# Optimization experiments

Measured on AMD Instinct MI355X. Metric: run time of the kernel, lower is better.

Reference implementation:

```python
import jax, jax.numpy as jnp
import numpy as np

B, V, M, H = 256, 128, 256, 1024
TIMING_DIM = 10          # ceil(log2(max_timesteps=1024))
DECAY_ALPHA = 0.99
IN_DIM = (V + TIMING_DIM + 1 + 1) * M  # 35840


def setup_inputs() -> dict:
    key = jax.random.key(0)
    ks = jax.random.split(key, 12)
    x = jax.random.uniform(ks[0], (B, V), dtype=jnp.float32)
    memory = jax.random.uniform(ks[1], (B, M, V), dtype=jnp.float32)
    memory_timings = jax.random.randint(ks[2], (B, M), 0, 1000).astype(jnp.int64)
    memory_surprise = jax.random.uniform(ks[3], (B, M), dtype=jnp.float32)
    last_prediction = jax.random.uniform(ks[4], (B, V), dtype=jnp.float32)
    s1 = 1.0 / np.sqrt(IN_DIM)
    s2 = 1.0 / np.sqrt(H)
    W1 = jax.random.uniform(ks[5], (IN_DIM, H), dtype=jnp.float32, minval=-s1, maxval=s1)
    b1 = jnp.zeros((H,), jnp.float32)
    Wg = jax.random.uniform(ks[6], (IN_DIM, H), dtype=jnp.float32, minval=-s1, maxval=s1)
    bg = jnp.zeros((H,), jnp.float32)
    W2 = jax.random.uniform(ks[7], (H, V), dtype=jnp.float32, minval=-s2, maxval=s2)
    b2 = jnp.zeros((V,), jnp.float32)
    return {"x": x, "memory": memory, "memory_timings": memory_timings,
            "memory_surprise": memory_surprise, "last_prediction": last_prediction,
            "W1": W1, "b1": b1, "Wg": Wg, "bg": bg, "W2": W2, "b2": b2}


def _step(x, memory, memory_timings, memory_surprise, last_prediction):
    # surprise of incoming token under last prediction
    surprise = -jnp.log(jnp.sum(x * last_prediction, axis=1) + 1e-8)  # [B]
    # age + decay
    timings = memory_timings + 1
    surp = memory_surprise * DECAY_ALPHA
    # ring-buffer roll, write newest at slot 0
    mem = jnp.roll(memory, 1, axis=1).at[:, 0, :].set(x)
    timings = jnp.roll(timings, 1, axis=1).at[:, 0].set(0)
    surp = jnp.roll(surp, 1, axis=1).at[:, 0].set(surprise)
    # sort by age ascending, gather memory/surprise
    idx = jnp.argsort(timings, axis=1)                               # [B,M]
    sorted_timings = jnp.take_along_axis(timings, idx, axis=1)       # [B,M]
    sorted_memory = jnp.take_along_axis(mem, idx[..., None], axis=1)  # [B,M,V]
    sorted_surprise = jnp.take_along_axis(surp, idx, axis=1)          # [B,M]
    # binary encode timings
    powers = 2 ** jnp.arange(TIMING_DIM, dtype=sorted_timings.dtype)
    bits = ((sorted_timings[..., None] // powers) % 2).astype(jnp.float32)  # [B,M,T]
    norm_t = sorted_timings.astype(jnp.float32) / (
        jnp.max(sorted_timings, axis=1, keepdims=True).astype(jnp.float32) + 1.0)
    pred_input = jnp.concatenate(
        [sorted_memory.reshape(B, -1), bits.reshape(B, -1),
         norm_t.reshape(B, -1), sorted_surprise.reshape(B, -1)], axis=1)  # [B, IN_DIM]
    return pred_input


def reference(x, memory, memory_timings, memory_surprise, last_prediction,
              W1, b1, Wg, bg, W2, b2):
    pred_input = _step(x, memory, memory_timings, memory_surprise, last_prediction)
    # gated dense network: h = (xW1+b1) * sigmoid(xWg+bg); logits = hW2+b2
    h = (pred_input @ W1 + b1) * jax.nn.sigmoid(pred_input @ Wg + bg)
    return h @ W2 + b2
```

## Files before the change

### kernel.cpp

```cpp
#include <hip/hip_runtime.h>
#include <stdint.h>
#include <math.h>

#define BB 256
#define VV 128
#define MM 256
#define TDIM 10
#define HH 1024
#define IN_DIM 35840
#define KSPLIT 16
#define KSLICE 2240
#define BK 32
#define NCHUNK 70

using f32x4  = __attribute__((ext_vector_type(4))) float;
using bf16x8 = __attribute__((ext_vector_type(8))) short;

__device__ __forceinline__ unsigned short f2bf(float f) {
    unsigned int u = __float_as_uint(f);
    unsigned int r = (u + 0x7FFFu + ((u >> 16) & 1u)) >> 16;
    return (unsigned short)r;
}

__device__ __forceinline__ void gload_lds16(const void* g, void* l) {
    __builtin_amdgcn_global_load_lds(
        (const __attribute__((address_space(1))) unsigned int*)g,
        (__attribute__((address_space(3))) unsigned int*)l,
        16, 0, 0);
}

__global__ __launch_bounds__(256)
void k_build(const float* __restrict__ x, const float* __restrict__ memory,
             const int* __restrict__ timings, const float* __restrict__ msurp,
             const float* __restrict__ lastp, short* __restrict__ A)
{
    int b = blockIdx.x, t = threadIdx.x;
    __shared__ int t_s[MM], idx_s[MM], st_s[MM];
    __shared__ float red[MM];
    __shared__ float s_surprise;

    t_s[t] = (t == 0) ? 0 : timings[b*MM + t - 1] + 1;
    red[t] = (t < VV) ? x[b*VV + t] * lastp[b*VV + t] : 0.f;
    __syncthreads();
    for (int s = 128; s > 0; s >>= 1) {
        if (t < s) red[t] += red[t + s];
        __syncthreads();
    }
    if (t == 0) s_surprise = -logf(red[0] + 1e-8f);

    int ti = t_s[t], cnt = 0;
    #pragma unroll 4
    for (int j = 0; j < MM; ++j) {
        int tj = t_s[j];
        cnt += (tj < ti) || (tj == ti && j < t);
    }
    idx_s[cnt] = t;
    st_s[cnt]  = ti;
    __syncthreads();

    float invm = 1.f / ((float)st_s[MM-1] + 1.f);
    short* Ab = A + (size_t)b * IN_DIM;
    {
        int st = st_s[t], src = idx_s[t];
        #pragma unroll
        for (int tt = 0; tt < TDIM; ++tt)
            Ab[32768 + t*TDIM + tt] = (short)f2bf((float)((st >> tt) & 1));
        Ab[35328 + t] = (short)f2bf((float)st * invm);
        float sv = (src == 0) ? s_surprise : msurp[b*MM + src - 1] * 0.99f;
        Ab[35584 + t] = (short)f2bf(sv);
    }
    int half = t >> 7, v = t & (VV-1);
    for (int p = half; p < MM; p += 2) {
        int src = idx_s[p];
        float val = (src == 0) ? x[b*VV + v]
                               : memory[((size_t)b*MM + src - 1)*VV + v];
        Ab[p*VV + v] = (short)f2bf(val);
    }
}

__global__ __launch_bounds__(512, 4)
void k_gemm(const short* __restrict__ A, const float* __restrict__ W1,
            const float* __restrict__ Wg, float* __restrict__ P)
{
    int ks = blockIdx.x;
    int xt = blockIdx.y;
    const float* W = (xt < 16) ? W1 : Wg;
    int wcol0 = (xt & 15) * 64;
    int pcol0 = xt * 64;
    int k0 = ks * KSLICE;

    __shared__ bf16x8 As8[3][1024];
    __shared__ float  Wl[3][2048];

    int t = threadIdx.x;
    int l = t & 63, wv = t >> 6;
    int r = l & 15, q = l >> 4;
    int wm = wv & 3, nh = wv >> 2;

    int aoff[4];
    #pragma unroll
    for (int mt = 0; mt < 4; ++mt) {
        int R = wm*64 + mt*16 + r;
        aoff[mt] = R*4 + (q ^ ((R >> 1) & 3));
    }
    int ncol[2];
    #pragma unroll
    for (int nt = 0; nt < 2; ++nt) {
        int n = nh*32 + nt*16 + r;
        ncol[nt] = n ^ (q << 4);
    }

    f32x4 acc[4][2];
    #pragma unroll
    for (int mt = 0; mt < 4; ++mt)
        #pragma unroll
        for (int nt = 0; nt < 2; ++nt)
            acc[mt][nt] = (f32x4){0.f, 0.f, 0.f, 0.f};

    int wkk = t >> 4;
    int wnF = ((t & 15) * 4) ^ (((wkk >> 3) & 3) << 4);

#define STAGE(sbuf, cc) do {                                                  \
        int kc_ = k0 + (cc)*BK;                                               \
        {   int G_ = t;                                                       \
            int m_ = G_ >> 2;                                                 \
            int kb_ = (G_ & 3) ^ ((m_ >> 1) & 3);                             \
            gload_lds16(A + (size_t)m_*IN_DIM + kc_ + kb_*8,                  \
                        (char*)&As8[sbuf][0] + (size_t)(t & ~63)*16);         \
        }                                                                     \
        {   int G_ = t + 512;                                                 \
            int m_ = G_ >> 2;                                                 \
            int kb_ = (G_ & 3) ^ ((m_ >> 1) & 3);                             \
            gload_lds16(A + (size_t)m_*IN_DIM + kc_ + kb_*8,                  \
                        (char*)&As8[sbuf][0] + (size_t)((t & ~63) + 512)*16); \
        }                                                                     \
        gload_lds16(W + (size_t)(kc_ + wkk)*HH + wcol0 + wnF,                 \
                    (char*)&Wl[sbuf][0] + (size_t)(t & ~63)*16);              \
    } while (0)

    STAGE(0, 0);
    STAGE(1, 1);
    STAGE(2, 2);
    asm volatile("s_waitcnt vmcnt(6)" ::: "memory");
    __builtin_amdgcn_s_barrier();

    for (int c = 0; c < NCHUNK; ++c) {
        int buf = c % 3;

        bf16x8 af[4], bfr[2];
        #pragma unroll
        for (int mt = 0; mt < 4; ++mt) af[mt] = As8[buf][aoff[mt]];
        #pragma unroll
        for (int nt = 0; nt < 2; ++nt) {
            const float* wb = &Wl[buf][ncol[nt]];
            bf16x8 bb;
            #pragma unroll
            for (int j = 0; j < 8; ++j)
                bb[j] = (short)f2bf(wb[(q*8 + j)*64]);
            bfr[nt] = bb;
        }
        #pragma unroll
        for (int mt = 0; mt < 4; ++mt)
            #pragma unroll
            for (int nt = 0; nt < 2; ++nt)
                acc[mt][nt] = __builtin_amdgcn_mfma_f32_16x16x32_bf16(
                    af[mt], bfr[nt], acc[mt][nt], 0, 0, 0);

        __builtin_amdgcn_s_barrier();
        {
            int cn = (c + 3 < NCHUNK) ? c + 3 : NCHUNK - 1;
            STAGE(buf, cn);
        }
        asm volatile("s_waitcnt vmcnt(6)" ::: "memory");
        __builtin_amdgcn_s_barrier();
    }
#undef STAGE

    #pragma unroll
    for (int mt = 0; mt < 4; ++mt)
        #pragma unroll
        for (int nt = 0; nt < 2; ++nt)
            #pragma unroll
            for (int rg = 0; rg < 4; ++rg) {
                int m = wm*64 + mt*16 + q*4 + rg;
                int n = pcol0 + nh*32 + nt*16 + r;
                P[((size_t)ks*BB + m)*2048 + n] = acc[mt][nt][rg];
            }
}

__global__ __launch_bounds__(256)
void k_reduce(const float* __restrict__ P, const float* __restrict__ b1,
              const float* __restrict__ bg, float* __restrict__ h)
{
    int b = blockIdx.x, t = threadIdx.x;
    const f32x4* P4 = (const f32x4*)P;
    f32x4 p1 = ((const f32x4*)b1)[t];
    f32x4 pg = ((const f32x4*)bg)[t];
    #pragma unroll
    for (int ks = 0; ks < KSPLIT; ++ks) {
        size_t base = ((size_t)ks*BB + b) * 512;
        p1 += P4[base + t];
        pg += P4[base + 256 + t];
    }
    f32x4 o;
    #pragma unroll
    for (int j = 0; j < 4; ++j)
        o[j] = p1[j] / (1.f + expf(-pg[j]));
    ((f32x4*)h)[(size_t)b*256 + t] = o;
}

__global__ __launch_bounds__(256)
void k_out(const float* __restrict__ h, const float* __restrict__ W2,
           const float* __restrict__ b2, float* __restrict__ out)
{
    int b = blockIdx.x, t = threadIdx.x;
    int v = t & 127, kh = t >> 7;
    const float* hb = h + (size_t)b*HH + kh*512;
    const float* wp = W2 + (size_t)kh*512*VV + v;
    float acc = 0.f;
    #pragma unroll 8
    for (int k = 0; k < 512; ++k)
        acc += hb[k] * wp[(size_t)k*VV];
    __shared__ float s[256];
    s[t] = acc;
    __syncthreads();
    if (t < 128)
        out[(size_t)b*VV + v] = s[t] + s[t + 128] + b2[v];
}

extern "C" void kernel_launch(void* const* d_in, const int* in_sizes, int n_in,
                              void* d_out, int out_size, void* d_ws, size_t ws_size,
                              hipStream_t stream)
{
    const float* x    = (const float*)d_in[0];
    const float* mem  = (const float*)d_in[1];
    const int*   tim  = (const int*)d_in[2];
    const float* msur = (const float*)d_in[3];
    const float* lp   = (const float*)d_in[4];
    const float* W1   = (const float*)d_in[5];
    const float* b1   = (const float*)d_in[6];
    const float* Wg   = (const float*)d_in[7];
    const float* bg   = (const float*)d_in[8];
    const float* W2   = (const float*)d_in[9];
    const float* b2   = (const float*)d_in[10];
    float* out = (float*)d_out;

    short* A = (short*)d_ws;
    float* P = (float*)((char*)d_ws + 18350080);
    float* h = (float*)((char*)d_ws + 51904512);

    k_build <<<256, 256, 0, stream>>>(x, mem, tim, msur, lp, A);
    k_gemm  <<<dim3(KSPLIT, 32), 512, 0, stream>>>(A, W1, Wg, P);
    k_reduce<<<256, 256, 0, stream>>>(P, b1, bg, h);
    k_out   <<<256, 256, 0, stream>>>(h, W2, b2, out);
}
```

Baseline: 431.8 us.

## Stage W through registers as bf16 MFMA-layout LDS tiles with register prefetch

Result: slower. 445.0 us (+3.1%).

```diff
diff --git a/kernel.cpp b/kernel.cpp
--- a/kernel.cpp
+++ b/kernel.cpp
@@ -90,24 +90,23 @@
     int k0 = ks * KSLICE;
 
     __shared__ bf16x8 As8[3][1024];
-    __shared__ float  Wl[3][2048];
+    __shared__ bf16x8 Ws8[2][256];
 
     int t = threadIdx.x;
     int l = t & 63, wv = t >> 6;
     int r = l & 15, q = l >> 4;
     int wm = wv & 3, nh = wv >> 2;
 
-    int aoff[4];
+    int aoff[4], boff[2];
     #pragma unroll
     for (int mt = 0; mt < 4; ++mt) {
         int R = wm*64 + mt*16 + r;
         aoff[mt] = R*4 + (q ^ ((R >> 1) & 3));
     }
-    int ncol[2];
     #pragma unroll
     for (int nt = 0; nt < 2; ++nt) {
-        int n = nh*32 + nt*16 + r;
-        ncol[nt] = n ^ (q << 4);
+        int R = nh*32 + nt*16 + r;
+        boff[nt] = R*4 + (q ^ ((R >> 1) & 3));
     }
 
     f32x4 acc[4][2];
@@ -117,64 +116,85 @@
         for (int nt = 0; nt < 2; ++nt)
             acc[mt][nt] = (f32x4){0.f, 0.f, 0.f, 0.f};
 
-    int wkk = t >> 4;
-    int wnF = ((t & 15) * 4) ^ (((wkk >> 3) & 3) << 4);
-
-#define STAGE(sbuf, cc) do {                                                  \
+    int wn = l;
+    int wkg = wv >> 1, whalf = wv & 1;
+    int wslot16 = (wn*4 + (wkg ^ ((wn >> 1) & 3))) * 16 + whalf * 8;
+    const float* wbase = W + (size_t)(k0 + wv*4)*HH + wcol0 + wn;
+
+#define STAGE_A(sbuf, cc) do {                                                \
         int kc_ = k0 + (cc)*BK;                                               \
         {   int G_ = t;                                                       \
             int m_ = G_ >> 2;                                                 \
             int kb_ = (G_ & 3) ^ ((m_ >> 1) & 3);                             \
             gload_lds16(A + (size_t)m_*IN_DIM + kc_ + kb_*8,                  \
-                        (char*)&As8[sbuf][0] + (size_t)(t & ~63)*16);         \
+                        (void*)(&As8[sbuf][0] + (t & ~63)));                  \
         }                                                                     \
         {   int G_ = t + 512;                                                 \
             int m_ = G_ >> 2;                                                 \
             int kb_ = (G_ & 3) ^ ((m_ >> 1) & 3);                             \
             gload_lds16(A + (size_t)m_*IN_DIM + kc_ + kb_*8,                  \
-                        (char*)&As8[sbuf][0] + (size_t)((t & ~63) + 512)*16); \
+                        (void*)(&As8[sbuf][0] + (t & ~63) + 512));            \
         }                                                                     \
-        gload_lds16(W + (size_t)(kc_ + wkk)*HH + wcol0 + wnF,                 \
-                    (char*)&Wl[sbuf][0] + (size_t)(t & ~63)*16);              \
-    } while (0)
-
-    STAGE(0, 0);
-    STAGE(1, 1);
-    STAGE(2, 2);
-    asm volatile("s_waitcnt vmcnt(6)" ::: "memory");
+    } while (0)
+
+#define WCONV(wreg, wdst) do {                                                \
+        unsigned int lo_ = (unsigned int)f2bf(wreg[0])                        \
+                         | ((unsigned int)f2bf(wreg[1]) << 16);               \
+        unsigned int hi_ = (unsigned int)f2bf(wreg[2])                        \
+                         | ((unsigned int)f2bf(wreg[3]) << 16);               \
+        unsigned int* d_ = (unsigned int*)((char*)&Ws8[wdst][0] + wslot16);   \
+        d_[0] = lo_; d_[1] = hi_;                                             \
+    } while (0)
+
+#define WLOAD(wreg, cc) do {                                                  \
+        const float* wp_ = wbase + (size_t)(cc)*BK*HH;                        \
+        _Pragma("unroll")                                                     \
+        for (int j_ = 0; j_ < 4; ++j_) wreg[j_] = wp_[(size_t)j_*HH];         \
+    } while (0)
+
+    float wA[4], wB[4], w0[4];
+
+    WLOAD(w0, 0);
+    STAGE_A(0, 0);
+    STAGE_A(1, 1);
+    WLOAD(wA, 1);
+    WCONV(w0, 0);
+    asm volatile("s_waitcnt vmcnt(0) lgkmcnt(0)" ::: "memory");
     __builtin_amdgcn_s_barrier();
 
-    for (int c = 0; c < NCHUNK; ++c) {
-        int buf = c % 3;
-
-        bf16x8 af[4], bfr[2];
-        #pragma unroll
-        for (int mt = 0; mt < 4; ++mt) af[mt] = As8[buf][aoff[mt]];
-        #pragma unroll
-        for (int nt = 0; nt < 2; ++nt) {
-            const float* wb = &Wl[buf][ncol[nt]];
-            bf16x8 bb;
-            #pragma unroll
-            for (int j = 0; j < 8; ++j)
-                bb[j] = (short)f2bf(wb[(q*8 + j)*64]);
-            bfr[nt] = bb;
-        }
-        #pragma unroll
-        for (int mt = 0; mt < 4; ++mt)
-            #pragma unroll
-            for (int nt = 0; nt < 2; ++nt)
-                acc[mt][nt] = __builtin_amdgcn_mfma_f32_16x16x32_bf16(
-                    af[mt], bfr[nt], acc[mt][nt], 0, 0, 0);
-
-        __builtin_amdgcn_s_barrier();
-        {
-            int cn = (c + 3 < NCHUNK) ? c + 3 : NCHUNK - 1;
-            STAGE(buf, cn);
-        }
-        asm volatile("s_waitcnt vmcnt(6)" ::: "memory");
-        __builtin_amdgcn_s_barrier();
-    }
-#undef STAGE
+#define CHUNK(c, WCUR, WNXT) do {                                             \
+        int pb_ = (c) % 3;                                                    \
+        int wrd_ = (c) & 1;                                                   \
+        int cN_ = ((c) + 2 < NCHUNK) ? (c) + 2 : NCHUNK - 1;                  \
+        STAGE_A(((c) + 2) % 3, cN_);                                          \
+        WLOAD(WNXT, cN_);                                                     \
+        {                                                                     \
+            bf16x8 af_[4], bf_[2];                                            \
+            _Pragma("unroll")                                                 \
+            for (int mt = 0; mt < 4; ++mt) af_[mt] = As8[pb_][aoff[mt]];      \
+            _Pragma("unroll")                                                 \
+            for (int nt = 0; nt < 2; ++nt) bf_[nt] = Ws8[wrd_][boff[nt]];     \
+            _Pragma("unroll")                                                 \
+            for (int mt = 0; mt < 4; ++mt)                                    \
+                _Pragma("unroll")                                             \
+                for (int nt = 0; nt < 2; ++nt)                                \
+                    acc[mt][nt] = __builtin_amdgcn_mfma_f32_16x16x32_bf16(    \
+                        af_[mt], bf_[nt], acc[mt][nt], 0, 0, 0);              \
+        }                                                                     \
+        WCONV(WCUR, wrd_ ^ 1);                                                \
+        asm volatile("s_waitcnt vmcnt(6) lgkmcnt(0)" ::: "memory");           \
+        __builtin_amdgcn_s_barrier();                                         \
+    } while (0)
+
+    #pragma unroll 1
+    for (int c = 0; c < NCHUNK; c += 2) {
+        CHUNK(c,     wA, wB);
+        CHUNK(c + 1, wB, wA);
+    }
+#undef CHUNK
+#undef WLOAD
+#undef WCONV
+#undef STAGE_A
 
     #pragma unroll
     for (int mt = 0; mt < 4; ++mt)
```

## Fuse split-K reduce with output GEMV and widen build kernel

Applied to the files above, without the earlier changes.

Result: faster. 403.0 us (-6.7%).

```diff
diff --git a/kernel.cpp b/kernel.cpp
--- a/kernel.cpp
+++ b/kernel.cpp
@@ -29,38 +29,41 @@
         16, 0, 0);
 }
 
-__global__ __launch_bounds__(256)
+__global__ __launch_bounds__(512)
 void k_build(const float* __restrict__ x, const float* __restrict__ memory,
              const int* __restrict__ timings, const float* __restrict__ msurp,
              const float* __restrict__ lastp, short* __restrict__ A)
 {
     int b = blockIdx.x, t = threadIdx.x;
     __shared__ int t_s[MM], idx_s[MM], st_s[MM];
-    __shared__ float red[MM];
     __shared__ float s_surprise;
 
-    t_s[t] = (t == 0) ? 0 : timings[b*MM + t - 1] + 1;
-    red[t] = (t < VV) ? x[b*VV + t] * lastp[b*VV + t] : 0.f;
-    __syncthreads();
-    for (int s = 128; s > 0; s >>= 1) {
-        if (t < s) red[t] += red[t + s];
-        __syncthreads();
-    }
-    if (t == 0) s_surprise = -logf(red[0] + 1e-8f);
-
-    int ti = t_s[t], cnt = 0;
-    #pragma unroll 4
-    for (int j = 0; j < MM; ++j) {
-        int tj = t_s[j];
-        cnt += (tj < ti) || (tj == ti && j < t);
-    }
-    idx_s[cnt] = t;
-    st_s[cnt]  = ti;
-    __syncthreads();
-
-    float invm = 1.f / ((float)st_s[MM-1] + 1.f);
+    if (t < MM) t_s[t] = (t == 0) ? 0 : timings[b*MM + t - 1] + 1;
+    if (t < 64) {
+        float v = x[b*VV + t] * lastp[b*VV + t]
+                + x[b*VV + t + 64] * lastp[b*VV + t + 64];
+        #pragma unroll
+        for (int off = 32; off > 0; off >>= 1)
+            v += __shfl_down(v, off, 64);
+        if (t == 0) s_surprise = -logf(v + 1e-8f);
+    }
+    __syncthreads();
+
+    if (t < MM) {
+        int ti = t_s[t], cnt = 0;
+        #pragma unroll 4
+        for (int j = 0; j < MM; ++j) {
+            int tj = t_s[j];
+            cnt += (tj < ti) || (tj == ti && j < t);
+        }
+        idx_s[cnt] = t;
+        st_s[cnt]  = ti;
+    }
+    __syncthreads();
+
     short* Ab = A + (size_t)b * IN_DIM;
-    {
+    if (t < MM) {
+        float invm = 1.f / ((float)st_s[MM-1] + 1.f);
         int st = st_s[t], src = idx_s[t];
         #pragma unroll
         for (int tt = 0; tt < TDIM; ++tt)
@@ -69,11 +72,15 @@
         float sv = (src == 0) ? s_surprise : msurp[b*MM + src - 1] * 0.99f;
         Ab[35584 + t] = (short)f2bf(sv);
     }
-    int half = t >> 7, v = t & (VV-1);
-    for (int p = half; p < MM; p += 2) {
+
+    int q4 = t >> 7, v = t & (VV-1);
+    float xv = x[b*VV + v];
+    #pragma unroll 8
+    for (int p = q4; p < MM; p += 4) {
         int src = idx_s[p];
-        float val = (src == 0) ? x[b*VV + v]
-                               : memory[((size_t)b*MM + src - 1)*VV + v];
+        int row = (src == 0) ? 0 : src - 1;
+        float mv = memory[((size_t)b*MM + row)*VV + v];
+        float val = (src == 0) ? xv : mv;
         Ab[p*VV + v] = (short)f2bf(val);
     }
 }
@@ -188,44 +195,46 @@
             }
 }
 
-__global__ __launch_bounds__(256)
-void k_reduce(const float* __restrict__ P, const float* __restrict__ b1,
-              const float* __restrict__ bg, float* __restrict__ h)
+__global__ __launch_bounds__(512)
+void k_tail(const float* __restrict__ P, const float* __restrict__ b1,
+            const float* __restrict__ bg, const float* __restrict__ W2,
+            const float* __restrict__ b2, float* __restrict__ out)
 {
     int b = blockIdx.x, t = threadIdx.x;
+    __shared__ f32x4 part[512];
+    __shared__ float hs[HH];
+    __shared__ float s2[512];
+
     const f32x4* P4 = (const f32x4*)P;
-    f32x4 p1 = ((const f32x4*)b1)[t];
-    f32x4 pg = ((const f32x4*)bg)[t];
-    #pragma unroll
-    for (int ks = 0; ks < KSPLIT; ++ks) {
-        size_t base = ((size_t)ks*BB + b) * 512;
-        p1 += P4[base + t];
-        pg += P4[base + 256 + t];
-    }
-    f32x4 o;
-    #pragma unroll
-    for (int j = 0; j < 4; ++j)
-        o[j] = p1[j] / (1.f + expf(-pg[j]));
-    ((f32x4*)h)[(size_t)b*256 + t] = o;
-}
-
-__global__ __launch_bounds__(256)
-void k_out(const float* __restrict__ h, const float* __restrict__ W2,
-           const float* __restrict__ b2, float* __restrict__ out)
-{
-    int b = blockIdx.x, t = threadIdx.x;
+    f32x4 s = (f32x4){0.f, 0.f, 0.f, 0.f};
+    #pragma unroll
+    for (int ks = 0; ks < KSPLIT; ++ks)
+        s += P4[((size_t)ks*BB + b)*512 + t];
+    part[t] = s;
+    __syncthreads();
+
+    if (t < 256) {
+        f32x4 p1 = part[t]       + ((const f32x4*)b1)[t];
+        f32x4 pg = part[t + 256] + ((const f32x4*)bg)[t];
+        f32x4 o;
+        #pragma unroll
+        for (int j = 0; j < 4; ++j)
+            o[j] = p1[j] / (1.f + expf(-pg[j]));
+        ((f32x4*)hs)[t] = o;
+    }
+    __syncthreads();
+
     int v = t & 127, kh = t >> 7;
-    const float* hb = h + (size_t)b*HH + kh*512;
-    const float* wp = W2 + (size_t)kh*512*VV + v;
+    const float* wp = W2 + (size_t)kh*256*VV + v;
+    const float* hk = hs + kh*256;
     float acc = 0.f;
     #pragma unroll 8
-    for (int k = 0; k < 512; ++k)
-        acc += hb[k] * wp[(size_t)k*VV];
-    __shared__ float s[256];
-    s[t] = acc;
+    for (int k = 0; k < 256; ++k)
+        acc += hk[k] * wp[(size_t)k*VV];
+    s2[t] = acc;
     __syncthreads();
     if (t < 128)
-        out[(size_t)b*VV + v] = s[t] + s[t + 128] + b2[v];
+        out[(size_t)b*VV + v] = s2[t] + s2[t+128] + s2[t+256] + s2[t+384] + b2[v];
 }
 
 extern "C" void kernel_launch(void* const* d_in, const int* in_sizes, int n_in,
@@ -247,10 +256,8 @@
 
     short* A = (short*)d_ws;
     float* P = (float*)((char*)d_ws + 18350080);
-    float* h = (float*)((char*)d_ws + 51904512);
-
-    k_build <<<256, 256, 0, stream>>>(x, mem, tim, msur, lp, A);
+
+    k_build <<<256, 512, 0, stream>>>(x, mem, tim, msur, lp, A);
     k_gemm  <<<dim3(KSPLIT, 32), 512, 0, stream>>>(A, W1, Wg, P);
-    k_reduce<<<256, 256, 0, stream>>>(P, b1, bg, h);
-    k_out   <<<256, 256, 0, stream>>>(h, W2, b2, out);
-}
+    k_tail  <<<256, 512, 0, stream>>>(P, b1, bg, W2, b2, out);
+}
```
